# Kernel optimization log

Hardware: AMD Instinct MI355X
Metric: run time of the kernel (lower is better)

## Reference

```python
import jax, jax.numpy as jnp
import numpy as np

N_NODES = 128
N_EDGES = N_NODES * (N_NODES - 1)  # fully-connected, no self-loops
N_IN = 128
N_HID = 256
N_OUT = 128
BATCH = 32


def _build_rel_matrices():
    # one-hot incidence matrices for fully-connected off-diagonal graph
    send_idx, recv_idx = [], []
    for i in range(N_NODES):
        for j in range(N_NODES):
            if i != j:
                send_idx.append(i)
                recv_idx.append(j)
    eye = np.eye(N_NODES, dtype=np.float32)
    rel_send = eye[np.asarray(send_idx)]  # [E, N]
    rel_rec = eye[np.asarray(recv_idx)]   # [E, N]
    return jnp.asarray(rel_rec), jnp.asarray(rel_send)


def setup_inputs() -> dict:
    key = jax.random.key(0)
    k = jax.random.split(key, 6)
    rel_rec, rel_send = _build_rel_matrices()
    s1 = 1.0 / np.sqrt(2 * N_IN)
    s2 = 1.0 / np.sqrt(N_HID)
    return {
        "x": jax.random.normal(k[0], (BATCH, N_NODES, N_IN), dtype=jnp.float32),
        "rel_type": jax.random.uniform(k[1], (BATCH, N_EDGES, 4), dtype=jnp.float32),
        "rel_rec": rel_rec,
        "rel_send": rel_send,
        "W1": jax.random.normal(k[2], (2 * N_IN, N_HID), dtype=jnp.float32) * s1,
        "b1": jnp.zeros((N_HID,), dtype=jnp.float32),
        "W2": jax.random.normal(k[3], (N_HID, N_OUT), dtype=jnp.float32) * s2,
        "b2": jnp.zeros((N_OUT,), dtype=jnp.float32),
    }


def reference(x, rel_type, rel_rec, rel_send, W1, b1, W2, b2):
    # node2edge: gather sender/receiver node features via incidence matmuls
    senders = jnp.einsum('en,bnf->bef', rel_send, x)    # [B, E, n_in]
    receivers = jnp.einsum('en,bnf->bef', rel_rec, x)   # [B, E, n_in]
    edges = jnp.concatenate([senders, receivers], axis=-1)  # [B, E, 2*n_in]
    # 2-layer MLP on edges (rel_type is unused in the original forward)
    h = jax.nn.relu(edges @ W1 + b1)
    msg = h @ W2 + b2                                   # [B, E, n_out]
    # edge2node: scatter-sum then normalize by in-degree
    agg = jnp.einsum('en,bef->bnf', rel_rec, msg)       # [B, N, n_out]
    norm = rel_rec.sum(axis=0)[None, :, None]           # [1, N, 1]
    return agg / (norm + 1e-6)
```

## Files before the change

kernel.cpp:

```cpp
#include <hip/hip_runtime.h>

#define BATCH 32
#define NN    128
#define NIN   128
#define NHID  256
#define NOUT  128
#define ROWS  (BATCH * NN)

__global__ __launch_bounds__(256) void k1_sr(
    const float* __restrict__ x, const float* __restrict__ W1,
    const float* __restrict__ b1, float* __restrict__ S, float* __restrict__ R)
{
    __shared__ float xr[8][128];
    const int row0 = blockIdx.x * 8;
    const int t = threadIdx.x;
    for (int idx = t; idx < 8 * 128; idx += 256)
        xr[idx >> 7][idx & 127] = x[(size_t)row0 * NIN + idx];
    __syncthreads();

    const int c = t;
    float accs[8], accr[8];
#pragma unroll
    for (int r = 0; r < 8; ++r) { accs[r] = 0.f; accr[r] = 0.f; }

    for (int k = 0; k < NIN; k += 4) {
        float wa[4], wb[4];
#pragma unroll
        for (int kk = 0; kk < 4; ++kk) {
            wa[kk] = W1[(size_t)(k + kk) * NHID + c];
            wb[kk] = W1[(size_t)(NIN + k + kk) * NHID + c];
        }
#pragma unroll
        for (int r = 0; r < 8; ++r) {
            const float4 xv = *(const float4*)(&xr[r][k]);
            accs[r] = fmaf(xv.w, wa[3], fmaf(xv.z, wa[2], fmaf(xv.y, wa[1], fmaf(xv.x, wa[0], accs[r]))));
            accr[r] = fmaf(xv.w, wb[3], fmaf(xv.z, wb[2], fmaf(xv.y, wb[1], fmaf(xv.x, wb[0], accr[r]))));
        }
    }
    const float bias = b1[c];
#pragma unroll
    for (int r = 0; r < 8; ++r) {
        S[(size_t)(row0 + r) * NHID + c] = accs[r];
        R[(size_t)(row0 + r) * NHID + c] = accr[r] + bias;
    }
}

__global__ __launch_bounds__(256) void k2_g(
    const float* __restrict__ S, const float* __restrict__ R, float* __restrict__ G)
{
    const int blk = blockIdx.x;
    const int b   = blk >> 4;
    const int nt  = (blk >> 2) & 3;
    const int cc  = blk & 3;
    const int c0  = cc * 64;

    __shared__ float s_lds[128][64];
    const int t  = threadIdx.x;
    const int cl = t & 63;
    const int ng = t >> 6;

    for (int idx = t; idx < 128 * 64; idx += 256) {
        const int i = idx >> 6, c = idx & 63;
        s_lds[i][c] = S[((size_t)(b * NN + i)) * NHID + c0 + c];
    }
    __syncthreads();

    const int n0 = nt * 32 + ng * 8;
    float rv[8], acc[8];
#pragma unroll
    for (int q = 0; q < 8; ++q) {
        rv[q]  = R[((size_t)(b * NN + n0 + q)) * NHID + c0 + cl];
        acc[q] = 0.f;
    }

    for (int i = 0; i < 128; ++i) {
        const float s = s_lds[i][cl];
#pragma unroll
        for (int q = 0; q < 8; ++q)
            acc[q] += fmaxf(s + rv[q], 0.f);
    }

#pragma unroll
    for (int q = 0; q < 8; ++q) {
        const float self = fmaxf(s_lds[n0 + q][cl] + rv[q], 0.f);
        G[((size_t)(b * NN + n0 + q)) * NHID + c0 + cl] = acc[q] - self;
    }
}

__global__ __launch_bounds__(256) void k3_out(
    const float* __restrict__ G, const float* __restrict__ W2,
    const float* __restrict__ b2, float* __restrict__ out)
{
    __shared__ float g[16][256];
    const int row0 = blockIdx.x * 16;
    const int t = threadIdx.x;
    for (int idx = t; idx < 16 * 256; idx += 256)
        g[idx >> 8][idx & 255] = G[(size_t)row0 * NHID + idx];
    __syncthreads();

    const int c  = t & 127;
    const int rh = t >> 7;
    float acc[8];
#pragma unroll
    for (int r = 0; r < 8; ++r) acc[r] = 0.f;

    for (int k = 0; k < NHID; k += 4) {
        float w[4];
#pragma unroll
        for (int kk = 0; kk < 4; ++kk)
            w[kk] = W2[(size_t)(k + kk) * NOUT + c];
#pragma unroll
        for (int r = 0; r < 8; ++r) {
            const float4 gv = *(const float4*)(&g[rh * 8 + r][k]);
            acc[r] = fmaf(gv.w, w[3], fmaf(gv.z, w[2], fmaf(gv.y, w[1], fmaf(gv.x, w[0], acc[r]))));
        }
    }
    const float inv  = 1.0f / (127.0f + 1e-6f);
    const float bias = 127.0f * b2[c];
#pragma unroll
    for (int r = 0; r < 8; ++r)
        out[(size_t)(row0 + rh * 8 + r) * NOUT + c] = (acc[r] + bias) * inv;
}

extern "C" void kernel_launch(void* const* d_in, const int* in_sizes, int n_in,
                              void* d_out, int out_size, void* d_ws, size_t ws_size,
                              hipStream_t stream)
{
    const float* x  = (const float*)d_in[0];
    const float* W1 = (const float*)d_in[4];
    const float* b1 = (const float*)d_in[5];
    const float* W2 = (const float*)d_in[6];
    const float* b2 = (const float*)d_in[7];
    float* out = (float*)d_out;

    float* S = (float*)d_ws;
    float* R = S + (size_t)ROWS * NHID;
    float* G = R + (size_t)ROWS * NHID;

    k1_sr <<<ROWS / 8,        256, 0, stream>>>(x, W1, b1, S, R);
    k2_g  <<<BATCH * 4 * 4,   256, 0, stream>>>(S, R, G);
    k3_out<<<ROWS / 16,       256, 0, stream>>>(G, W2, b2, out);
}
```

Before: 121.6 us.

## Fuse relu-aggregation and W2 projection into one kernel, drop G buffer

Merges the edge-aggregation kernel and the output-projection kernel into a single kernel. Each block handles 8 nodes of one batch and loops over four 64-column chunks of hidden features, computing the aggregated hidden values into LDS and immediately multiplying them by W2. This removes one launch and the global write and read of the G intermediate. In exchange, each block reloads the full S tile for its batch, so S is read 16 times per batch instead of 4 and S-loading work per block grows. Each thread also now does only 2 rows in the aggregation loop and 4 rows in the projection loop, which lowers the work per thread.

```diff
diff --git a/kernel.cpp b/kernel.cpp
--- a/kernel.cpp
+++ b/kernel.cpp
@@ -45,81 +45,70 @@
     }
 }
 
-__global__ __launch_bounds__(256) void k2_g(
-    const float* __restrict__ S, const float* __restrict__ R, float* __restrict__ G)
+__global__ __launch_bounds__(256) void kB(
+    const float* __restrict__ S, const float* __restrict__ R,
+    const float* __restrict__ W2, const float* __restrict__ b2,
+    float* __restrict__ out)
 {
+    __shared__ float s_lds[128][64];
+    __shared__ float g_lds[8][64];
     const int blk = blockIdx.x;
     const int b   = blk >> 4;
-    const int nt  = (blk >> 2) & 3;
-    const int cc  = blk & 3;
-    const int c0  = cc * 64;
+    const int nt  = blk & 15;
+    const int n0  = nt * 8;
+    const int t   = threadIdx.x;
+    const int cl  = t & 63;
+    const int rq  = t >> 6;
+    const int co  = t & 127;
+    const int rh  = t >> 7;
 
-    __shared__ float s_lds[128][64];
-    const int t  = threadIdx.x;
-    const int cl = t & 63;
-    const int ng = t >> 6;
+    const float4* S4 = (const float4*)S;
 
-    for (int idx = t; idx < 128 * 64; idx += 256) {
-        const int i = idx >> 6, c = idx & 63;
-        s_lds[i][c] = S[((size_t)(b * NN + i)) * NHID + c0 + c];
-    }
-    __syncthreads();
+    float acc[4] = {0.f, 0.f, 0.f, 0.f};
 
-    const int n0 = nt * 32 + ng * 8;
-    float rv[8], acc[8];
+    for (int cc = 0; cc < 4; ++cc) {
+        const int c0 = cc * 64;
+        __syncthreads();
+        for (int idx = t; idx < 2048; idx += 256) {
+            const int i = idx >> 4, j = idx & 15;
+            ((float4*)s_lds)[idx] = S4[(size_t)(b * NN + i) * 64 + cc * 16 + j];
+        }
+        float rv[2];
 #pragma unroll
-    for (int q = 0; q < 8; ++q) {
-        rv[q]  = R[((size_t)(b * NN + n0 + q)) * NHID + c0 + cl];
-        acc[q] = 0.f;
+        for (int q = 0; q < 2; ++q)
+            rv[q] = R[(size_t)(b * NN + n0 + rq * 2 + q) * NHID + c0 + cl];
+        __syncthreads();
+
+        float ag[2] = {0.f, 0.f};
+        for (int i = 0; i < 128; ++i) {
+            const float s = s_lds[i][cl];
+            ag[0] += fmaxf(s + rv[0], 0.f);
+            ag[1] += fmaxf(s + rv[1], 0.f);
+        }
+#pragma unroll
+        for (int q = 0; q < 2; ++q) {
+            const int lr = rq * 2 + q;
+            ag[q] -= fmaxf(s_lds[n0 + lr][cl] + rv[q], 0.f);
+            g_lds[lr][cl] = ag[q];
+        }
+        __syncthreads();
+
+        for (int k = 0; k < 64; k += 2) {
+            const float w0 = W2[(size_t)(c0 + k    ) * NOUT + co];
+            const float w1 = W2[(size_t)(c0 + k + 1) * NOUT + co];
+#pragma unroll
+            for (int r = 0; r < 4; ++r) {
+                acc[r] = fmaf(g_lds[rh * 4 + r][k],     w0, acc[r]);
+                acc[r] = fmaf(g_lds[rh * 4 + r][k + 1], w1, acc[r]);
+            }
+        }
     }
 
-    for (int i = 0; i < 128; ++i) {
-        const float s = s_lds[i][cl];
+    const float inv  = 1.0f / (127.0f + 1e-6f);
+    const float bias = 127.0f * b2[co];
 #pragma unroll
-        for (int q = 0; q < 8; ++q)
-            acc[q] += fmaxf(s + rv[q], 0.f);
-    }
-
-#pragma unroll
-    for (int q = 0; q < 8; ++q) {
-        const float self = fmaxf(s_lds[n0 + q][cl] + rv[q], 0.f);
-        G[((size_t)(b * NN + n0 + q)) * NHID + c0 + cl] = acc[q] - self;
-    }
-}
-
-__global__ __launch_bounds__(256) void k3_out(
-    const float* __restrict__ G, const float* __restrict__ W2,
-    const float* __restrict__ b2, float* __restrict__ out)
-{
-    __shared__ float g[16][256];
-    const int row0 = blockIdx.x * 16;
-    const int t = threadIdx.x;
-    for (int idx = t; idx < 16 * 256; idx += 256)
-        g[idx >> 8][idx & 255] = G[(size_t)row0 * NHID + idx];
-    __syncthreads();
-
-    const int c  = t & 127;
-    const int rh = t >> 7;
-    float acc[8];
-#pragma unroll
-    for (int r = 0; r < 8; ++r) acc[r] = 0.f;
-
-    for (int k = 0; k < NHID; k += 4) {
-        float w[4];
-#pragma unroll
-        for (int kk = 0; kk < 4; ++kk)
-            w[kk] = W2[(size_t)(k + kk) * NOUT + c];
-#pragma unroll
-        for (int r = 0; r < 8; ++r) {
-            const float4 gv = *(const float4*)(&g[rh * 8 + r][k]);
-            acc[r] = fmaf(gv.w, w[3], fmaf(gv.z, w[2], fmaf(gv.y, w[1], fmaf(gv.x, w[0], acc[r]))));
-        }
-    }
-    const float inv  = 1.0f / (127.0f + 1e-6f);
-    const float bias = 127.0f * b2[c];
-#pragma unroll
-    for (int r = 0; r < 8; ++r)
-        out[(size_t)(row0 + rh * 8 + r) * NOUT + c] = (acc[r] + bias) * inv;
+    for (int r = 0; r < 4; ++r)
+        out[(size_t)(b * NN + n0 + rh * 4 + r) * NOUT + co] = (acc[r] + bias) * inv;
 }
 
 extern "C" void kernel_launch(void* const* d_in, const int* in_sizes, int n_in,
@@ -135,9 +124,7 @@
 
     float* S = (float*)d_ws;
     float* R = S + (size_t)ROWS * NHID;
-    float* G = R + (size_t)ROWS * NHID;
 
-    k1_sr <<<ROWS / 8,        256, 0, stream>>>(x, W1, b1, S, R);
-    k2_g  <<<BATCH * 4 * 4,   256, 0, stream>>>(S, R, G);
-    k3_out<<<ROWS / 16,       256, 0, stream>>>(G, W2, b2, out);
+    k1_sr<<<ROWS / 8,  256, 0, stream>>>(x, W1, b1, S, R);
+    kB   <<<BATCH * 16, 256, 0, stream>>>(S, R, W2, b2, out);
 }
```

After: 127.2 us. 1.05x slower.

## Use float4 register tiles across all three kernels

Applied to the files above, without the earlier changes.

Each thread now computes a 4-column by several-row register tile using float4 loads of weights, inputs and outputs in all three kernels. The block-to-work mapping changes too: k1 handles 16 rows per block and k2 uses 256 blocks covering 64 nodes by 64 channels. The goal is fewer global load instructions, better vectorized memory traffic and more FMAs per LDS and global load. The trade-off is fewer blocks in k1 and k2, which lowers parallelism, plus more registers per thread, which can lower occupancy.

```diff
diff --git a/kernel.cpp b/kernel.cpp
--- a/kernel.cpp
+++ b/kernel.cpp
@@ -7,41 +7,55 @@
 #define NOUT  128
 #define ROWS  (BATCH * NN)
 
+__device__ __forceinline__ float4 fma4(float a, const float4 w, const float4 c) {
+    float4 r;
+    r.x = fmaf(a, w.x, c.x); r.y = fmaf(a, w.y, c.y);
+    r.z = fmaf(a, w.z, c.z); r.w = fmaf(a, w.w, c.w);
+    return r;
+}
+
 __global__ __launch_bounds__(256) void k1_sr(
     const float* __restrict__ x, const float* __restrict__ W1,
     const float* __restrict__ b1, float* __restrict__ S, float* __restrict__ R)
 {
-    __shared__ float xr[8][128];
-    const int row0 = blockIdx.x * 8;
+    __shared__ float xr[16][128];
+    const int row0 = blockIdx.x * 16;
     const int t = threadIdx.x;
-    for (int idx = t; idx < 8 * 128; idx += 256)
-        xr[idx >> 7][idx & 127] = x[(size_t)row0 * NIN + idx];
+    const float4* x4 = (const float4*)(x + (size_t)row0 * NIN);
+    float4* xr4 = (float4*)xr;
+    for (int idx = t; idx < 512; idx += 256) xr4[idx] = x4[idx];
     __syncthreads();
 
-    const int c = t;
-    float accs[8], accr[8];
+    const int c4 = (t & 63) * 4;
+    const int r0 = (t >> 6) * 4;
+    float4 accs[4], accr[4];
 #pragma unroll
-    for (int r = 0; r < 8; ++r) { accs[r] = 0.f; accr[r] = 0.f; }
+    for (int r = 0; r < 4; ++r) {
+        accs[r] = make_float4(0.f, 0.f, 0.f, 0.f);
+        accr[r] = make_float4(0.f, 0.f, 0.f, 0.f);
+    }
 
     for (int k = 0; k < NIN; k += 4) {
-        float wa[4], wb[4];
+        float4 wa[4], wb[4];
 #pragma unroll
         for (int kk = 0; kk < 4; ++kk) {
-            wa[kk] = W1[(size_t)(k + kk) * NHID + c];
-            wb[kk] = W1[(size_t)(NIN + k + kk) * NHID + c];
+            wa[kk] = *(const float4*)&W1[(size_t)(k + kk) * NHID + c4];
+            wb[kk] = *(const float4*)&W1[(size_t)(NIN + k + kk) * NHID + c4];
         }
 #pragma unroll
-        for (int r = 0; r < 8; ++r) {
-            const float4 xv = *(const float4*)(&xr[r][k]);
-            accs[r] = fmaf(xv.w, wa[3], fmaf(xv.z, wa[2], fmaf(xv.y, wa[1], fmaf(xv.x, wa[0], accs[r]))));
-            accr[r] = fmaf(xv.w, wb[3], fmaf(xv.z, wb[2], fmaf(xv.y, wb[1], fmaf(xv.x, wb[0], accr[r]))));
+        for (int r = 0; r < 4; ++r) {
+            const float4 xv = *(const float4*)(&xr[r0 + r][k]);
+            accs[r] = fma4(xv.x, wa[0], fma4(xv.y, wa[1], fma4(xv.z, wa[2], fma4(xv.w, wa[3], accs[r]))));
+            accr[r] = fma4(xv.x, wb[0], fma4(xv.y, wb[1], fma4(xv.z, wb[2], fma4(xv.w, wb[3], accr[r]))));
         }
     }
-    const float bias = b1[c];
+    const float4 bias = *(const float4*)&b1[c4];
 #pragma unroll
-    for (int r = 0; r < 8; ++r) {
-        S[(size_t)(row0 + r) * NHID + c] = accs[r];
-        R[(size_t)(row0 + r) * NHID + c] = accr[r] + bias;
+    for (int r = 0; r < 4; ++r) {
+        *(float4*)&S[(size_t)(row0 + r0 + r) * NHID + c4] = accs[r];
+        float4 rr = accr[r];
+        rr.x += bias.x; rr.y += bias.y; rr.z += bias.z; rr.w += bias.w;
+        *(float4*)&R[(size_t)(row0 + r0 + r) * NHID + c4] = rr;
     }
 }
 
@@ -49,41 +63,47 @@
     const float* __restrict__ S, const float* __restrict__ R, float* __restrict__ G)
 {
     const int blk = blockIdx.x;
-    const int b   = blk >> 4;
-    const int nt  = (blk >> 2) & 3;
-    const int cc  = blk & 3;
-    const int c0  = cc * 64;
+    const int b   = blk >> 3;
+    const int cc  = (blk >> 1) & 3;
+    const int rh  = blk & 1;
 
-    __shared__ float s_lds[128][64];
-    const int t  = threadIdx.x;
-    const int cl = t & 63;
-    const int ng = t >> 6;
+    __shared__ float4 s4[128 * 16];
+    const float4* S4 = (const float4*)S;
+    const float4* R4 = (const float4*)R;
+    float4*       G4 = (float4*)G;
+    const int t = threadIdx.x;
 
-    for (int idx = t; idx < 128 * 64; idx += 256) {
-        const int i = idx >> 6, c = idx & 63;
-        s_lds[i][c] = S[((size_t)(b * NN + i)) * NHID + c0 + c];
+    for (int idx = t; idx < 2048; idx += 256)
+        s4[idx] = S4[(size_t)(b * NN + (idx >> 4)) * 64 + cc * 16 + (idx & 15)];
+
+    const int cg = t & 15;
+    const int n0 = rh * 64 + (t >> 4) * 4;
+    float4 rv[4], acc[4];
+#pragma unroll
+    for (int q = 0; q < 4; ++q) {
+        rv[q]  = R4[(size_t)(b * NN + n0 + q) * 64 + cc * 16 + cg];
+        acc[q] = make_float4(0.f, 0.f, 0.f, 0.f);
     }
     __syncthreads();
 
-    const int n0 = nt * 32 + ng * 8;
-    float rv[8], acc[8];
+    for (int i = 0; i < 128; ++i) {
+        const float4 s = s4[i * 16 + cg];
 #pragma unroll
-    for (int q = 0; q < 8; ++q) {
-        rv[q]  = R[((size_t)(b * NN + n0 + q)) * NHID + c0 + cl];
-        acc[q] = 0.f;
+        for (int q = 0; q < 4; ++q) {
+            acc[q].x += fmaxf(s.x + rv[q].x, 0.f);
+            acc[q].y += fmaxf(s.y + rv[q].y, 0.f);
+            acc[q].z += fmaxf(s.z + rv[q].z, 0.f);
+            acc[q].w += fmaxf(s.w + rv[q].w, 0.f);
+        }
     }
-
-    for (int i = 0; i < 128; ++i) {
-        const float s = s_lds[i][cl];
 #pragma unroll
-        for (int q = 0; q < 8; ++q)
-            acc[q] += fmaxf(s + rv[q], 0.f);
-    }
-
-#pragma unroll
-    for (int q = 0; q < 8; ++q) {
-        const float self = fmaxf(s_lds[n0 + q][cl] + rv[q], 0.f);
-        G[((size_t)(b * NN + n0 + q)) * NHID + c0 + cl] = acc[q] - self;
+    for (int q = 0; q < 4; ++q) {
+        const float4 sq = s4[(n0 + q) * 16 + cg];
+        acc[q].x -= fmaxf(sq.x + rv[q].x, 0.f);
+        acc[q].y -= fmaxf(sq.y + rv[q].y, 0.f);
+        acc[q].z -= fmaxf(sq.z + rv[q].z, 0.f);
+        acc[q].w -= fmaxf(sq.w + rv[q].w, 0.f);
+        G4[(size_t)(b * NN + n0 + q) * 64 + cc * 16 + cg] = acc[q];
     }
 }
 
@@ -94,32 +114,40 @@
     __shared__ float g[16][256];
     const int row0 = blockIdx.x * 16;
     const int t = threadIdx.x;
-    for (int idx = t; idx < 16 * 256; idx += 256)
-        g[idx >> 8][idx & 255] = G[(size_t)row0 * NHID + idx];
+    const float4* Gg = (const float4*)(G + (size_t)row0 * NHID);
+    float4* g4 = (float4*)g;
+    for (int idx = t; idx < 1024; idx += 256) g4[idx] = Gg[idx];
     __syncthreads();
 
-    const int c  = t & 127;
-    const int rh = t >> 7;
-    float acc[8];
-#pragma unroll
-    for (int r = 0; r < 8; ++r) acc[r] = 0.f;
+    const int c4 = (t & 31) * 4;
+    const int r0 = (t >> 5) * 2;
+    float4 acc[2];
+    acc[0] = make_float4(0.f, 0.f, 0.f, 0.f);
+    acc[1] = make_float4(0.f, 0.f, 0.f, 0.f);
 
     for (int k = 0; k < NHID; k += 4) {
-        float w[4];
+        float4 w[4];
 #pragma unroll
         for (int kk = 0; kk < 4; ++kk)
-            w[kk] = W2[(size_t)(k + kk) * NOUT + c];
+            w[kk] = *(const float4*)&W2[(size_t)(k + kk) * NOUT + c4];
 #pragma unroll
-        for (int r = 0; r < 8; ++r) {
-            const float4 gv = *(const float4*)(&g[rh * 8 + r][k]);
-            acc[r] = fmaf(gv.w, w[3], fmaf(gv.z, w[2], fmaf(gv.y, w[1], fmaf(gv.x, w[0], acc[r]))));
+        for (int r = 0; r < 2; ++r) {
+            const float4 gv = *(const float4*)(&g[r0 + r][k]);
+            acc[r] = fma4(gv.x, w[0], fma4(gv.y, w[1], fma4(gv.z, w[2], fma4(gv.w, w[3], acc[r]))));
         }
     }
-    const float inv  = 1.0f / (127.0f + 1e-6f);
-    const float bias = 127.0f * b2[c];
+    const float inv = 1.0f / (127.0f + 1e-6f);
+    float4 bias = *(const float4*)&b2[c4];
+    bias.x *= 127.f; bias.y *= 127.f; bias.z *= 127.f; bias.w *= 127.f;
 #pragma unroll
-    for (int r = 0; r < 8; ++r)
-        out[(size_t)(row0 + rh * 8 + r) * NOUT + c] = (acc[r] + bias) * inv;
+    for (int r = 0; r < 2; ++r) {
+        float4 o;
+        o.x = (acc[r].x + bias.x) * inv;
+        o.y = (acc[r].y + bias.y) * inv;
+        o.z = (acc[r].z + bias.z) * inv;
+        o.w = (acc[r].w + bias.w) * inv;
+        *(float4*)&out[(size_t)(row0 + r0 + r) * NOUT + c4] = o;
+    }
 }
 
 extern "C" void kernel_launch(void* const* d_in, const int* in_sizes, int n_in,
@@ -137,7 +165,7 @@
     float* R = S + (size_t)ROWS * NHID;
     float* G = R + (size_t)ROWS * NHID;
 
-    k1_sr <<<ROWS / 8,        256, 0, stream>>>(x, W1, b1, S, R);
-    k2_g  <<<BATCH * 4 * 4,   256, 0, stream>>>(S, R, G);
-    k3_out<<<ROWS / 16,       256, 0, stream>>>(G, W2, b2, out);
+    k1_sr <<<ROWS / 16, 256, 0, stream>>>(x, W1, b1, S, R);
+    k2_g  <<<256,       256, 0, stream>>>(S, R, G);
+    k3_out<<<ROWS / 16, 256, 0, stream>>>(G, W2, b2, out);
 }
```

Measured after the change: 176.3 us. 1.45x slower.
